# Optimization experiments

Hardware: AMD Instinct MI355X
Metric: run time of the kernel (lower is better)

Reference implementation:

```python
import jax, jax.numpy as jnp
import numpy as np

N, E, G, H, F_IN = 100_000, 3_200_000, 256, 16, 7
RRELU_SLOPE = (1.0 / 8.0 + 1.0 / 3.0) / 2.0  # eval-mode RReLU uses mean slope


def rrelu(x):
    return jnp.where(x >= 0, x, RRELU_SLOPE * x)


def gcn_conv(x, edge_index, edge_weight, W, b, n_nodes):
    """PyG GCNConv: add self-loops, symmetric norm, gather-matmul-scatter."""
    row, col = edge_index[0], edge_index[1]
    loop = jnp.arange(n_nodes)
    row = jnp.concatenate([row, loop])
    col = jnp.concatenate([col, loop])
    w = jnp.concatenate([edge_weight, jnp.ones((n_nodes,), x.dtype)])
    deg = jax.ops.segment_sum(w, col, num_segments=n_nodes)
    dis = jnp.where(deg > 0, jax.lax.rsqrt(jnp.maximum(deg, 1e-12)), 0.0)
    norm = dis[row] * w * dis[col]            # [E+N]
    h = x @ W                                  # [N, out]
    msg = h[row] * norm[:, None]               # gather + scale
    return jax.ops.segment_sum(msg, col, num_segments=n_nodes) + b


def max_pool_neighbor_x(x, edge_index, n_nodes):
    row, col = edge_index[0], edge_index[1]
    loop = jnp.arange(n_nodes)
    row = jnp.concatenate([row, loop])
    col = jnp.concatenate([col, loop])
    return jax.ops.segment_max(x[row], col, num_segments=n_nodes)


def setup_inputs() -> dict:
    key = jax.random.key(0)
    ks = jax.random.split(key, 12)
    x = jax.random.normal(ks[0], (N, F_IN), jnp.float32)
    edge_index = jax.random.randint(ks[1], (2, E), 0, N)
    edge_weights = jax.random.uniform(ks[2], (E,), jnp.float32)
    batch = (jnp.arange(N) * G) // N  # sorted, every graph non-empty
    s = 0.2
    W1 = jax.random.normal(ks[3], (F_IN, H), jnp.float32) * s
    b1 = jnp.zeros((H,), jnp.float32)
    W2 = jax.random.normal(ks[4], (H, H), jnp.float32) * s
    b2 = jnp.zeros((H,), jnp.float32)
    Wl1 = jax.random.normal(ks[5], (H, H), jnp.float32) * s
    bl1 = jax.random.normal(ks[6], (H,), jnp.float32) * s
    Wl3 = jax.random.normal(ks[7], (H, H), jnp.float32) * s
    bl3 = jax.random.normal(ks[8], (H,), jnp.float32) * s
    Wl4 = jax.random.normal(ks[9], (H, 1), jnp.float32) * s
    bl4 = jax.random.normal(ks[10], (1,), jnp.float32) * s
    return {"x": x, "edge_index": edge_index, "batch": batch,
            "edge_weights": edge_weights, "W1": W1, "b1": b1, "W2": W2,
            "b2": b2, "Wl1": Wl1, "bl1": bl1, "Wl3": Wl3, "bl3": bl3,
            "Wl4": Wl4, "bl4": bl4}


def reference(x, edge_index, batch, edge_weights, W1, b1, W2, b2,
              Wl1, bl1, Wl3, bl3, Wl4, bl4):
    h = gcn_conv(x, edge_index, edge_weights, W1, b1, N)
    h = max_pool_neighbor_x(h, edge_index, N)
    res = h
    h = gcn_conv(h, edge_index, jnp.ones((E,), h.dtype), W2, b2, N)
    h = jax.nn.relu(res + h)
    g = jax.ops.segment_max(h, batch, num_segments=G)  # global_max_pool
    res = g
    g = rrelu(res + (g @ Wl1 + bl1))
    res = g
    g = rrelu(res + (g @ Wl3 + bl3))
    # dropout p=0.5 in eval mode -> identity
    g = rrelu(g @ Wl4 + bl4)
    return g
```

## Files before the change

kernel.cpp:

```cpp
#include <hip/hip_runtime.h>
#include <hip/hip_fp16.h>
#include <math.h>

#define NN 100000
#define NE 3200000
#define NG 256
#define HD 16
#define FIN 7

#define RB 8
#define RSZ 256
#define NBUK 391
#define FB 1024
#define CHUNK 3125
#define ASTRIDE 17
#define CSTRIDE 9
#define LMASK 0x1FFFF

#define S16 65536.0f
#define INV_S16 1.52587890625e-5f
#define IBIAS 33554432u
#define S_DEGW 16777216.0f
#define INV_S_DEGW 5.9604644775390625e-8f

static constexpr float SLOPE = 0.22916666666666666f;

__device__ __forceinline__ float rrelu_f(float a) {
    return a >= 0.f ? a : SLOPE * a;
}

__device__ __forceinline__ unsigned encf(float v) {
    unsigned u = __float_as_uint(v);
    return u ^ (((unsigned)((int)u >> 31)) | 0x80000000u);
}
__device__ __forceinline__ float decf(unsigned u) {
    unsigned m = ((int)u < 0) ? 0x80000000u : 0xFFFFFFFFu;
    return __uint_as_float(u ^ m);
}
#define ENC_NEGINF 0x00800000u

__global__ __launch_bounds__(256) void k_node_prep(
        const float* __restrict__ x, const float* __restrict__ W1,
        float* __restrict__ h1) {
    int t = blockIdx.x * 256 + threadIdx.x;
    if (t >= NN * HD) return;
    int i = t >> 4, f = t & 15;
    float acc = 0.f;
#pragma unroll
    for (int k = 0; k < FIN; ++k) acc += x[i * FIN + k] * W1[k * HD + f];
    h1[t] = acc;
}

__global__ __launch_bounds__(256) void k_hist(
        const int* __restrict__ col, int* __restrict__ hist) {
    __shared__ int bins[NBUK];
    for (int i = threadIdx.x; i < NBUK; i += 256) bins[i] = 0;
    __syncthreads();
    int base = blockIdx.x * CHUNK;
    for (int i = threadIdx.x; i < CHUNK; i += 256)
        atomicAdd(&bins[col[base + i] >> RB], 1);
    __syncthreads();
    for (int i = threadIdx.x; i < NBUK; i += 256)
        hist[blockIdx.x * NBUK + i] = bins[i];
}

__global__ __launch_bounds__(FB) void k_scan_a(
        const int* __restrict__ hist, int* __restrict__ pre, int* __restrict__ tot) {
    __shared__ int s[FB];
    int t = threadIdx.x;
    int v = hist[t * NBUK + blockIdx.x];
    s[t] = v;
    __syncthreads();
    for (int d = 1; d < FB; d <<= 1) {
        int add = (t >= d) ? s[t - d] : 0;
        __syncthreads();
        s[t] += add;
        __syncthreads();
    }
    pre[blockIdx.x * FB + t] = s[t] - v;
    if (t == FB - 1) tot[blockIdx.x] = s[t];
}

__global__ __launch_bounds__(512) void k_scan_b(
        const int* __restrict__ tot, int* __restrict__ bstart) {
    __shared__ int s[512];
    int t = threadIdx.x;
    int v = (t < NBUK) ? tot[t] : 0;
    s[t] = v;
    __syncthreads();
    for (int d = 1; d < 512; d <<= 1) {
        int add = (t >= d) ? s[t - d] : 0;
        __syncthreads();
        s[t] += add;
        __syncthreads();
    }
    if (t < NBUK) bstart[t + 1] = s[t];
    if (t == 0) bstart[0] = 0;
}

__global__ __launch_bounds__(256) void k_fill(
        const int* __restrict__ row, const int* __restrict__ col,
        const float* __restrict__ ew,
        const int* __restrict__ pre, const int* __restrict__ bstart,
        uint2* __restrict__ spw) {
    __shared__ int lcnt[NBUK];
    __shared__ int gofs[NBUK];
    __shared__ int part[256];
    __shared__ unsigned short sbuk[CHUNK];
    __shared__ uint2 stage[CHUNK];
    int t = threadIdx.x;
    for (int i = t; i < NBUK; i += 256) {
        lcnt[i] = 0;
        gofs[i] = bstart[i] + pre[i * FB + blockIdx.x];
    }
    __syncthreads();
    int base = blockIdx.x * CHUNK;
    for (int i = t; i < CHUNK; i += 256)
        atomicAdd(&lcnt[col[base + i] >> RB], 1);
    __syncthreads();
    int k0 = t * 2;
    int c0 = (k0 + 0 < NBUK) ? lcnt[k0 + 0] : 0;
    int c1 = (k0 + 1 < NBUK) ? lcnt[k0 + 1] : 0;
    int gsum = c0 + c1;
    part[t] = gsum;
    __syncthreads();
    for (int d = 1; d < 256; d <<= 1) {
        int add = (t >= d) ? part[t - d] : 0;
        __syncthreads();
        part[t] += add;
        __syncthreads();
    }
    {
        int run = part[t] - gsum;
        int e0 = run, e1 = run + c0;
        if (k0 + 0 < NBUK) { gofs[k0 + 0] -= e0; lcnt[k0 + 0] = e0; }
        if (k0 + 1 < NBUK) { gofs[k0 + 1] -= e1; lcnt[k0 + 1] = e1; }
    }
    __syncthreads();
    for (int i = t; i < CHUNK; i += 256) {
        int c = col[base + i];
        int b = c >> RB;
        int s = atomicAdd(&lcnt[b], 1);
        stage[s] = make_uint2(((unsigned)(c & (RSZ - 1)) << 17) | (unsigned)row[base + i],
                              __float_as_uint(ew[base + i]));
        sbuk[s] = (unsigned short)b;
    }
    __syncthreads();
    for (int s = t; s < CHUNK; s += 256)
        spw[s + gofs[sbuk[s]]] = stage[s];
}

__global__ __launch_bounds__(1024) void k_deg(
        const uint2* __restrict__ spw, const int* __restrict__ bstart,
        const float* __restrict__ h1,
        float* __restrict__ dis1, float* __restrict__ dis2,
        int* __restrict__ cnts, unsigned* __restrict__ h1h) {
    __shared__ unsigned long long sdeg[RSZ];
    __shared__ float sdis[RSZ];
    int t = threadIdx.x;
    if (t < RSZ) sdeg[t] = 0ULL;
    __syncthreads();
    int s0 = bstart[blockIdx.x], s1 = bstart[blockIdx.x + 1];
    int j = s0 + t;
    for (; j + 3072 < s1; j += 4096) {
        uint2 e0 = spw[j], e1 = spw[j + 1024], e2 = spw[j + 2048], e3 = spw[j + 3072];
        atomicAdd(&sdeg[e0.x >> 17], (1ULL << 32) |
                  (unsigned long long)(unsigned)__float2int_rn(__uint_as_float(e0.y) * S_DEGW));
        atomicAdd(&sdeg[e1.x >> 17], (1ULL << 32) |
                  (unsigned long long)(unsigned)__float2int_rn(__uint_as_float(e1.y) * S_DEGW));
        atomicAdd(&sdeg[e2.x >> 17], (1ULL << 32) |
                  (unsigned long long)(unsigned)__float2int_rn(__uint_as_float(e2.y) * S_DEGW));
        atomicAdd(&sdeg[e3.x >> 17], (1ULL << 32) |
                  (unsigned long long)(unsigned)__float2int_rn(__uint_as_float(e3.y) * S_DEGW));
    }
    for (; j < s1; j += 1024) {
        uint2 e = spw[j];
        atomicAdd(&sdeg[e.x >> 17], (1ULL << 32) |
                  (unsigned long long)(unsigned)__float2int_rn(__uint_as_float(e.y) * S_DEGW));
    }
    __syncthreads();
    int node0 = blockIdx.x * RSZ;
    if (t < RSZ && node0 + t < NN) {
        unsigned long long v = sdeg[t];
        unsigned cnt = (unsigned)(v >> 32);
        float wsum = (float)(unsigned)(v & 0xFFFFFFFFULL) * INV_S_DEGW;
        float d1 = rsqrtf(wsum + 1.f);
        dis1[node0 + t] = d1;
        sdis[t] = d1;
        dis2[node0 + t] = rsqrtf((float)cnt + 1.f);
        cnts[node0 + t] = (int)cnt;
    }
    __syncthreads();
    for (int i = t; i < RSZ * 8; i += 1024) {
        int ln = i >> 3, p = i & 7;
        int node = node0 + ln;
        if (node < NN) {
            float d = sdis[ln];
            __half2 hh = __floats2half2_rn(h1[node * HD + 2 * p] * d,
                                           h1[node * HD + 2 * p + 1] * d);
            h1h[node * 8 + p] = *(unsigned*)&hh;
        }
    }
}

__device__ __forceinline__ void conv_acc(unsigned long long* acc, unsigned ex,
                                         unsigned g, float w, int p) {
    float2 f = __half22float2(*(__half2*)&g);
    unsigned q0 = (unsigned)__float2int_rn(f.x * w) + IBIAS;
    unsigned q1 = (unsigned)__float2int_rn(f.y * w) + IBIAS;
    atomicAdd(&acc[(ex >> 17) * CSTRIDE + p],
              ((unsigned long long)q0 << 32) | (unsigned long long)q1);
}

__global__ __launch_bounds__(1024) void k_conv1(
        const uint2* __restrict__ spw, const int* __restrict__ bstart,
        const unsigned* __restrict__ h1h, const float* __restrict__ h1,
        const float* __restrict__ dis1, const int* __restrict__ cnts,
        const float* __restrict__ b1, unsigned* __restrict__ h1outh) {
    __shared__ unsigned long long acc[RSZ * CSTRIDE];
    int t = threadIdx.x;
    for (int i = t; i < RSZ * CSTRIDE; i += 1024) acc[i] = 0ULL;
    __syncthreads();
    int p = t & 7, slot = t >> 3;
    int s0 = bstart[blockIdx.x], s1 = bstart[blockIdx.x + 1];
    int j = s0 + slot;
    for (; j + 384 < s1; j += 512) {
        uint2 e0 = spw[j], e1 = spw[j + 128], e2 = spw[j + 256], e3 = spw[j + 384];
        unsigned g0 = h1h[(e0.x & LMASK) * 8 + p];
        unsigned g1 = h1h[(e1.x & LMASK) * 8 + p];
        unsigned g2 = h1h[(e2.x & LMASK) * 8 + p];
        unsigned g3 = h1h[(e3.x & LMASK) * 8 + p];
        conv_acc(acc, e0.x, g0, __uint_as_float(e0.y) * S16, p);
        conv_acc(acc, e1.x, g1, __uint_as_float(e1.y) * S16, p);
        conv_acc(acc, e2.x, g2, __uint_as_float(e2.y) * S16, p);
        conv_acc(acc, e3.x, g3, __uint_as_float(e3.y) * S16, p);
    }
    for (; j < s1; j += 128) {
        uint2 e = spw[j];
        unsigned g = h1h[(e.x & LMASK) * 8 + p];
        conv_acc(acc, e.x, g, __uint_as_float(e.y) * S16, p);
    }
    __syncthreads();
    int node0 = blockIdx.x * RSZ;
    for (int i = t; i < RSZ * 8; i += 1024) {
        int ln = i >> 3, pp = i & 7;
        int node = node0 + ln;
        if (node < NN) {
            unsigned long long v = acc[ln * CSTRIDE + pp];
            unsigned kb = (unsigned)cnts[node] * IBIAS;
            float a0 = (float)(int)((unsigned)(v >> 32) - kb) * INV_S16;
            float a1 = (float)(int)((unsigned)(v & 0xFFFFFFFFULL) - kb) * INV_S16;
            float d = dis1[node];
            float r0 = a0 * d + h1[node * HD + 2 * pp] * d * d + b1[2 * pp];
            float r1 = a1 * d + h1[node * HD + 2 * pp + 1] * d * d + b1[2 * pp + 1];
            __half2 hh = __floats2half2_rn(r0, r1);
            h1outh[node * 8 + pp] = *(unsigned*)&hh;
        }
    }
}

__global__ __launch_bounds__(1024) void k_pool_h2(
        const uint2* __restrict__ spw, const int* __restrict__ bstart,
        const unsigned* __restrict__ h1outh, const float* __restrict__ W2,
        const float* __restrict__ dis2,
        float2* __restrict__ pool2, float2* __restrict__ h2s,
        unsigned* __restrict__ h2sh) {
    __shared__ unsigned acc[RSZ * ASTRIDE];
    __shared__ float sW2[256];
    int t = threadIdx.x;
    if (t < 256) sW2[t] = W2[t];
    for (int i = t; i < RSZ * ASTRIDE; i += 1024) acc[i] = ENC_NEGINF;
    __syncthreads();
    int p = t & 7, slot = t >> 3;
    int s0 = bstart[blockIdx.x], s1 = bstart[blockIdx.x + 1];
    int j = s0 + slot;
    for (; j + 384 < s1; j += 512) {
        unsigned e0 = spw[j].x, e1 = spw[j + 128].x, e2 = spw[j + 256].x, e3 = spw[j + 384].x;
        unsigned g0 = h1outh[(e0 & LMASK) * 8 + p];
        unsigned g1 = h1outh[(e1 & LMASK) * 8 + p];
        unsigned g2 = h1outh[(e2 & LMASK) * 8 + p];
        unsigned g3 = h1outh[(e3 & LMASK) * 8 + p];
        float2 f;
        f = __half22float2(*(__half2*)&g0);
        atomicMax(&acc[(e0 >> 17) * ASTRIDE + 2 * p], encf(f.x));
        atomicMax(&acc[(e0 >> 17) * ASTRIDE + 2 * p + 1], encf(f.y));
        f = __half22float2(*(__half2*)&g1);
        atomicMax(&acc[(e1 >> 17) * ASTRIDE + 2 * p], encf(f.x));
        atomicMax(&acc[(e1 >> 17) * ASTRIDE + 2 * p + 1], encf(f.y));
        f = __half22float2(*(__half2*)&g2);
        atomicMax(&acc[(e2 >> 17) * ASTRIDE + 2 * p], encf(f.x));
        atomicMax(&acc[(e2 >> 17) * ASTRIDE + 2 * p + 1], encf(f.y));
        f = __half22float2(*(__half2*)&g3);
        atomicMax(&acc[(e3 >> 17) * ASTRIDE + 2 * p], encf(f.x));
        atomicMax(&acc[(e3 >> 17) * ASTRIDE + 2 * p + 1], encf(f.y));
    }
    for (; j < s1; j += 128) {
        unsigned e = spw[j].x;
        unsigned g = h1outh[(e & LMASK) * 8 + p];
        float2 f = __half22float2(*(__half2*)&g);
        atomicMax(&acc[(e >> 17) * ASTRIDE + 2 * p], encf(f.x));
        atomicMax(&acc[(e >> 17) * ASTRIDE + 2 * p + 1], encf(f.y));
    }
    __syncthreads();
    int node0 = blockIdx.x * RSZ;
    for (int i = t; i < RSZ * 8; i += 1024) {
        int ln = i >> 3, pp = i & 7;
        int node = node0 + ln;
        if (node < NN) {
            unsigned sh = h1outh[node * 8 + pp];
            float2 sf = __half22float2(*(__half2*)&sh);
            float m0 = fmaxf(decf(acc[ln * ASTRIDE + 2 * pp]),     sf.x);
            float m1 = fmaxf(decf(acc[ln * ASTRIDE + 2 * pp + 1]), sf.y);
            pool2[node * 8 + pp] = make_float2(m0, m1);
            acc[ln * ASTRIDE + 2 * pp]     = __float_as_uint(m0);
            acc[ln * ASTRIDE + 2 * pp + 1] = __float_as_uint(m1);
        }
    }
    __syncthreads();
    for (int i = t; i < RSZ * 8; i += 1024) {
        int ln = i >> 3, pp = i & 7;
        int node = node0 + ln;
        if (node < NN) {
            float a0 = 0.f, a1 = 0.f;
#pragma unroll
            for (int k = 0; k < HD; ++k) {
                float pv = __uint_as_float(acc[ln * ASTRIDE + k]);
                a0 += pv * sW2[k * HD + 2 * pp];
                a1 += pv * sW2[k * HD + 2 * pp + 1];
            }
            float d = dis2[node];
            a0 *= d; a1 *= d;
            h2s[node * 8 + pp] = make_float2(a0, a1);
            __half2 hh = __floats2half2_rn(a0, a1);
            h2sh[node * 8 + pp] = *(unsigned*)&hh;
        }
    }
}

__global__ __launch_bounds__(1024) void k_conv2(
        const uint2* __restrict__ spw, const int* __restrict__ bstart,
        const unsigned* __restrict__ h2sh, const float2* __restrict__ h2s,
        const float* __restrict__ dis2, const int* __restrict__ cnts,
        const float2* __restrict__ pool2, const float* __restrict__ b2,
        float2* __restrict__ hfin2) {
    __shared__ unsigned long long acc[RSZ * CSTRIDE];
    int t = threadIdx.x;
    for (int i = t; i < RSZ * CSTRIDE; i += 1024) acc[i] = 0ULL;
    __syncthreads();
    int p = t & 7, slot = t >> 3;
    int s0 = bstart[blockIdx.x], s1 = bstart[blockIdx.x + 1];
    int j = s0 + slot;
    for (; j + 384 < s1; j += 512) {
        unsigned e0 = spw[j].x, e1 = spw[j + 128].x, e2 = spw[j + 256].x, e3 = spw[j + 384].x;
        unsigned g0 = h2sh[(e0 & LMASK) * 8 + p];
        unsigned g1 = h2sh[(e1 & LMASK) * 8 + p];
        unsigned g2 = h2sh[(e2 & LMASK) * 8 + p];
        unsigned g3 = h2sh[(e3 & LMASK) * 8 + p];
        conv_acc(acc, e0, g0, S16, p);
        conv_acc(acc, e1, g1, S16, p);
        conv_acc(acc, e2, g2, S16, p);
        conv_acc(acc, e3, g3, S16, p);
    }
    for (; j < s1; j += 128) {
        unsigned e = spw[j].x;
        unsigned g = h2sh[(e & LMASK) * 8 + p];
        conv_acc(acc, e, g, S16, p);
    }
    __syncthreads();
    int node0 = blockIdx.x * RSZ;
    for (int i = t; i < RSZ * 8; i += 1024) {
        int ln = i >> 3, pp = i & 7;
        int node = node0 + ln;
        if (node < NN) {
            unsigned long long v = acc[ln * CSTRIDE + pp];
            unsigned kb = (unsigned)cnts[node] * IBIAS;
            float a0 = (float)(int)((unsigned)(v >> 32) - kb) * INV_S16;
            float a1 = (float)(int)((unsigned)(v & 0xFFFFFFFFULL) - kb) * INV_S16;
            float d = dis2[node];
            float2 self = h2s[node * 8 + pp];
            float2 pl = pool2[node * 8 + pp];
            float r0 = pl.x + (a0 + self.x) * d + b2[2 * pp];
            float r1 = pl.y + (a1 + self.y) * d + b2[2 * pp + 1];
            hfin2[node * 8 + pp] = make_float2(fmaxf(r0, 0.f), fmaxf(r1, 0.f));
        }
    }
}

__global__ __launch_bounds__(256) void k_graph_max(
        const float* __restrict__ hfin, float* __restrict__ gbuf) {
    int g = blockIdx.x;
    int start = (g * NN + NG - 1) / NG;
    int end   = ((g + 1) * NN + NG - 1) / NG;
    int f = threadIdx.x & 15, sub = threadIdx.x >> 4;
    float m = -3.402823466e38f;
    for (int i = start + sub; i < end; i += 16)
        m = fmaxf(m, hfin[i * HD + f]);
    __shared__ float lds[256];
    lds[threadIdx.x] = m;
    __syncthreads();
    if (threadIdx.x < 16) {
        float mm = lds[threadIdx.x];
#pragma unroll
        for (int s = 1; s < 16; ++s) mm = fmaxf(mm, lds[s * 16 + threadIdx.x]);
        gbuf[g * HD + threadIdx.x] = mm;
    }
}

__global__ __launch_bounds__(256) void k_mlp(
        const float* __restrict__ gbuf,
        const float* __restrict__ Wl1, const float* __restrict__ bl1,
        const float* __restrict__ Wl3, const float* __restrict__ bl3,
        const float* __restrict__ Wl4, const float* __restrict__ bl4,
        float* __restrict__ out) {
    __shared__ float sW1[256], sW3[256], sW4[16], sb1[16], sb3[16];
    __shared__ float sb4;
    int tid = threadIdx.x;
    sW1[tid] = Wl1[tid];
    sW3[tid] = Wl3[tid];
    if (tid < 16) { sW4[tid] = Wl4[tid]; sb1[tid] = bl1[tid]; sb3[tid] = bl3[tid]; }
    if (tid == 0) sb4 = bl4[0];
    __syncthreads();

    float v[16], t1[16], t2[16];
#pragma unroll
    for (int f = 0; f < 16; ++f) v[f] = gbuf[tid * 16 + f];
#pragma unroll
    for (int f = 0; f < 16; ++f) {
        float a = sb1[f] + v[f];
#pragma unroll
        for (int k = 0; k < 16; ++k) a += v[k] * sW1[k * 16 + f];
        t1[f] = rrelu_f(a);
    }
#pragma unroll
    for (int f = 0; f < 16; ++f) {
        float a = sb3[f] + t1[f];
#pragma unroll
        for (int k = 0; k < 16; ++k) a += t1[k] * sW3[k * 16 + f];
        t2[f] = rrelu_f(a);
    }
    float o = sb4;
#pragma unroll
    for (int k = 0; k < 16; ++k) o += t2[k] * sW4[k];
    out[tid] = rrelu_f(o);
}

extern "C" void kernel_launch(void* const* d_in, const int* in_sizes, int n_in,
                              void* d_out, int out_size, void* d_ws, size_t ws_size,
                              hipStream_t stream) {
    const float* x   = (const float*)d_in[0];
    const int*   ei  = (const int*)  d_in[1];
    const float* ew  = (const float*)d_in[3];
    const float* W1  = (const float*)d_in[4];
    const float* b1  = (const float*)d_in[5];
    const float* W2  = (const float*)d_in[6];
    const float* b2  = (const float*)d_in[7];
    const float* Wl1 = (const float*)d_in[8];
    const float* bl1 = (const float*)d_in[9];
    const float* Wl3 = (const float*)d_in[10];
    const float* bl3 = (const float*)d_in[11];
    const float* Wl4 = (const float*)d_in[12];
    const float* bl4 = (const float*)d_in[13];
    const int* row = ei;
    const int* col = ei + NE;

    float* ws = (float*)d_ws;
    float* h1    = ws;
    float* pool  = h1   + NN * HD;
    float* h2s   = pool + NN * HD;
    float* dis1  = h2s  + NN * HD;
    float* dis2  = dis1 + NN;
    int*   cnts  = (int*)(dis2 + NN);
    float* gbuf  = (float*)(cnts + NN);
    unsigned* h1h    = (unsigned*)(gbuf + NG * HD);
    unsigned* h1outh = h1h    + NN * 8;
    unsigned* h2sh   = h1outh + NN * 8;
    uint2*    spw    = (uint2*)(h2sh + NN * 8);
    int* tot    = (int*)(spw + NE);
    int* bstart = tot + NBUK;
    int* hist   = (int*)pool;
    int* pre    = (int*)h2s;
    float* hfin = h1;

    const int B = 256;

    k_node_prep<<<(NN * HD + B - 1) / B, B, 0, stream>>>(x, W1, h1);
    k_hist     <<<FB, B, 0, stream>>>(col, hist);
    k_scan_a   <<<NBUK, FB, 0, stream>>>(hist, pre, tot);
    k_scan_b   <<<1, 512, 0, stream>>>(tot, bstart);
    k_fill     <<<FB, B, 0, stream>>>(row, col, ew, pre, bstart, spw);
    k_deg      <<<NBUK, 1024, 0, stream>>>(spw, bstart, h1, dis1, dis2, cnts, h1h);
    k_conv1    <<<NBUK, 1024, 0, stream>>>(spw, bstart, h1h, h1, dis1, cnts, b1, h1outh);
    k_pool_h2  <<<NBUK, 1024, 0, stream>>>(spw, bstart, h1outh, W2, dis2,
                                           (float2*)pool, (float2*)h2s, h2sh);
    k_conv2    <<<NBUK, 1024, 0, stream>>>(spw, bstart, h2sh, (const float2*)h2s, dis2,
                                           cnts, (const float2*)pool, b2, (float2*)hfin);
    k_graph_max<<<NG, B, 0, stream>>>(hfin, gbuf);
    k_mlp      <<<1, B, 0, stream>>>(gbuf, Wl1, bl1, Wl3, bl3, Wl4, bl4, (float*)d_out);
}
```

Baseline: 266.4 us.

## Split edge records into index and fp16 weight arrays, widen gathers, fuse node prep

Stores sorted edges as a 32-bit packed index array plus a separate fp16 weight array instead of 8-byte uint2 records, shrinking edge traffic in every pass (conv2 and pool no longer read weights at all). Gather kernels now have each thread load 8-byte uint2 feature chunks (4 threads per edge) and issue paired atomics. The x@W1 node prep is fused into k_deg, and the bucket scan is rewritten to process 8 columns per block with a transposed layout and wavefront shuffles. Converting edge weights to fp16 adds rounding error to degrees and messages.

```diff
diff --git a/kernel.cpp b/kernel.cpp
--- a/kernel.cpp
+++ b/kernel.cpp
@@ -11,8 +11,10 @@
 #define RB 8
 #define RSZ 256
 #define NBUK 391
+#define NBUKP 400
 #define FB 1024
 #define CHUNK 3125
+#define SCB 8
 #define ASTRIDE 17
 #define CSTRIDE 9
 #define LMASK 0x1FFFF
@@ -39,16 +41,9 @@
 }
 #define ENC_NEGINF 0x00800000u
 
-__global__ __launch_bounds__(256) void k_node_prep(
-        const float* __restrict__ x, const float* __restrict__ W1,
-        float* __restrict__ h1) {
-    int t = blockIdx.x * 256 + threadIdx.x;
-    if (t >= NN * HD) return;
-    int i = t >> 4, f = t & 15;
-    float acc = 0.f;
-#pragma unroll
-    for (int k = 0; k < FIN; ++k) acc += x[i * FIN + k] * W1[k * HD + f];
-    h1[t] = acc;
+__device__ __forceinline__ float h2f(unsigned short us) {
+    __half h = *(__half*)&us;
+    return __half2float(h);
 }
 
 __global__ __launch_bounds__(256) void k_hist(
@@ -61,24 +56,47 @@
         atomicAdd(&bins[col[base + i] >> RB], 1);
     __syncthreads();
     for (int i = threadIdx.x; i < NBUK; i += 256)
-        hist[blockIdx.x * NBUK + i] = bins[i];
-}
-
-__global__ __launch_bounds__(FB) void k_scan_a(
-        const int* __restrict__ hist, int* __restrict__ pre, int* __restrict__ tot) {
-    __shared__ int s[FB];
-    int t = threadIdx.x;
-    int v = hist[t * NBUK + blockIdx.x];
-    s[t] = v;
-    __syncthreads();
-    for (int d = 1; d < FB; d <<= 1) {
-        int add = (t >= d) ? s[t - d] : 0;
-        __syncthreads();
-        s[t] += add;
-        __syncthreads();
-    }
-    pre[blockIdx.x * FB + t] = s[t] - v;
-    if (t == FB - 1) tot[blockIdx.x] = s[t];
+        hist[blockIdx.x * NBUKP + i] = bins[i];
+}
+
+__global__ __launch_bounds__(512) void k_scan_a(
+        const int* __restrict__ hist, int* __restrict__ pre_t,
+        int* __restrict__ tot) {
+    __shared__ int s[SCB * (FB + 1)];
+    int t = threadIdx.x;
+    int c0 = blockIdx.x * SCB;
+    for (int i = t; i < SCB * FB; i += 512) {
+        int j = i >> 3, c = i & 7;
+        int cc = c0 + c;
+        s[c * (FB + 1) + j] = (cc < NBUK) ? hist[j * NBUKP + cc] : 0;
+    }
+    __syncthreads();
+    int w = t >> 6, l = t & 63;
+    int* sb = &s[w * (FB + 1)];
+    int base = l * 16;
+    int loc[16];
+    int run = 0;
+#pragma unroll
+    for (int k = 0; k < 16; ++k) { loc[k] = run; run += sb[base + k]; }
+    int inc = run;
+#pragma unroll
+    for (int d = 1; d < 64; d <<= 1) {
+        int v = __shfl_up(inc, d, 64);
+        if (l >= d) inc += v;
+    }
+    int excl = inc - run;
+    int cc = c0 + w;
+    if (cc < NBUK) {
+#pragma unroll
+        for (int k = 0; k < 16; ++k) sb[base + k] = excl + loc[k];
+        if (l == 63) tot[cc] = inc;
+    }
+    __syncthreads();
+    for (int i = t; i < SCB * FB; i += 512) {
+        int j = i >> 3, c = i & 7;
+        int cc2 = c0 + c;
+        if (cc2 < NBUK) pre_t[j * NBUKP + cc2] = s[c * (FB + 1) + j];
+    }
 }
 
 __global__ __launch_bounds__(512) void k_scan_b(
@@ -101,17 +119,18 @@
 __global__ __launch_bounds__(256) void k_fill(
         const int* __restrict__ row, const int* __restrict__ col,
         const float* __restrict__ ew,
-        const int* __restrict__ pre, const int* __restrict__ bstart,
-        uint2* __restrict__ spw) {
+        const int* __restrict__ pre_t, const int* __restrict__ bstart,
+        unsigned* __restrict__ sp, unsigned short* __restrict__ swh) {
     __shared__ int lcnt[NBUK];
     __shared__ int gofs[NBUK];
     __shared__ int part[256];
+    __shared__ unsigned ssp[CHUNK];
+    __shared__ unsigned short ssw[CHUNK];
     __shared__ unsigned short sbuk[CHUNK];
-    __shared__ uint2 stage[CHUNK];
     int t = threadIdx.x;
     for (int i = t; i < NBUK; i += 256) {
         lcnt[i] = 0;
-        gofs[i] = bstart[i] + pre[i * FB + blockIdx.x];
+        gofs[i] = bstart[i] + pre_t[blockIdx.x * NBUKP + i];
     }
     __syncthreads();
     int base = blockIdx.x * CHUNK;
@@ -141,42 +160,53 @@
         int c = col[base + i];
         int b = c >> RB;
         int s = atomicAdd(&lcnt[b], 1);
-        stage[s] = make_uint2(((unsigned)(c & (RSZ - 1)) << 17) | (unsigned)row[base + i],
-                              __float_as_uint(ew[base + i]));
+        ssp[s] = ((unsigned)(c & (RSZ - 1)) << 17) | (unsigned)row[base + i];
+        __half hv = __float2half_rn(ew[base + i]);
+        ssw[s] = *(unsigned short*)&hv;
         sbuk[s] = (unsigned short)b;
     }
     __syncthreads();
-    for (int s = t; s < CHUNK; s += 256)
-        spw[s + gofs[sbuk[s]]] = stage[s];
+    for (int s = t; s < CHUNK; s += 256) {
+        int g = s + gofs[sbuk[s]];
+        sp[g] = ssp[s];
+        swh[g] = ssw[s];
+    }
 }
 
 __global__ __launch_bounds__(1024) void k_deg(
-        const uint2* __restrict__ spw, const int* __restrict__ bstart,
-        const float* __restrict__ h1,
-        float* __restrict__ dis1, float* __restrict__ dis2,
-        int* __restrict__ cnts, unsigned* __restrict__ h1h) {
+        const unsigned* __restrict__ sp, const unsigned short* __restrict__ swh,
+        const int* __restrict__ bstart,
+        const float* __restrict__ x, const float* __restrict__ W1,
+        float* __restrict__ h1, float* __restrict__ dis1,
+        float* __restrict__ dis2, int* __restrict__ cnts,
+        unsigned* __restrict__ h1h) {
     __shared__ unsigned long long sdeg[RSZ];
     __shared__ float sdis[RSZ];
-    int t = threadIdx.x;
+    __shared__ float sW1[FIN * HD];
+    int t = threadIdx.x;
+    if (t < FIN * HD) sW1[t] = W1[t];
     if (t < RSZ) sdeg[t] = 0ULL;
     __syncthreads();
     int s0 = bstart[blockIdx.x], s1 = bstart[blockIdx.x + 1];
     int j = s0 + t;
     for (; j + 3072 < s1; j += 4096) {
-        uint2 e0 = spw[j], e1 = spw[j + 1024], e2 = spw[j + 2048], e3 = spw[j + 3072];
-        atomicAdd(&sdeg[e0.x >> 17], (1ULL << 32) |
-                  (unsigned long long)(unsigned)__float2int_rn(__uint_as_float(e0.y) * S_DEGW));
-        atomicAdd(&sdeg[e1.x >> 17], (1ULL << 32) |
-                  (unsigned long long)(unsigned)__float2int_rn(__uint_as_float(e1.y) * S_DEGW));
-        atomicAdd(&sdeg[e2.x >> 17], (1ULL << 32) |
-                  (unsigned long long)(unsigned)__float2int_rn(__uint_as_float(e2.y) * S_DEGW));
-        atomicAdd(&sdeg[e3.x >> 17], (1ULL << 32) |
-                  (unsigned long long)(unsigned)__float2int_rn(__uint_as_float(e3.y) * S_DEGW));
+        unsigned e0 = sp[j], e1 = sp[j + 1024], e2 = sp[j + 2048], e3 = sp[j + 3072];
+        float w0 = h2f(swh[j]), w1 = h2f(swh[j + 1024]);
+        float w2 = h2f(swh[j + 2048]), w3 = h2f(swh[j + 3072]);
+        atomicAdd(&sdeg[e0 >> 17], (1ULL << 32) |
+                  (unsigned long long)(unsigned)__float2int_rn(w0 * S_DEGW));
+        atomicAdd(&sdeg[e1 >> 17], (1ULL << 32) |
+                  (unsigned long long)(unsigned)__float2int_rn(w1 * S_DEGW));
+        atomicAdd(&sdeg[e2 >> 17], (1ULL << 32) |
+                  (unsigned long long)(unsigned)__float2int_rn(w2 * S_DEGW));
+        atomicAdd(&sdeg[e3 >> 17], (1ULL << 32) |
+                  (unsigned long long)(unsigned)__float2int_rn(w3 * S_DEGW));
     }
     for (; j < s1; j += 1024) {
-        uint2 e = spw[j];
-        atomicAdd(&sdeg[e.x >> 17], (1ULL << 32) |
-                  (unsigned long long)(unsigned)__float2int_rn(__uint_as_float(e.y) * S_DEGW));
+        unsigned e = sp[j];
+        float w = h2f(swh[j]);
+        atomicAdd(&sdeg[e >> 17], (1ULL << 32) |
+                  (unsigned long long)(unsigned)__float2int_rn(w * S_DEGW));
     }
     __syncthreads();
     int node0 = blockIdx.x * RSZ;
@@ -195,25 +225,40 @@
         int ln = i >> 3, p = i & 7;
         int node = node0 + ln;
         if (node < NN) {
+            float a0 = 0.f, a1 = 0.f;
+#pragma unroll
+            for (int k = 0; k < FIN; ++k) {
+                float xv = x[node * FIN + k];
+                a0 += xv * sW1[k * HD + 2 * p];
+                a1 += xv * sW1[k * HD + 2 * p + 1];
+            }
+            h1[node * HD + 2 * p] = a0;
+            h1[node * HD + 2 * p + 1] = a1;
             float d = sdis[ln];
-            __half2 hh = __floats2half2_rn(h1[node * HD + 2 * p] * d,
-                                           h1[node * HD + 2 * p + 1] * d);
+            __half2 hh = __floats2half2_rn(a0 * d, a1 * d);
             h1h[node * 8 + p] = *(unsigned*)&hh;
         }
     }
 }
 
-__device__ __forceinline__ void conv_acc(unsigned long long* acc, unsigned ex,
-                                         unsigned g, float w, int p) {
-    float2 f = __half22float2(*(__half2*)&g);
-    unsigned q0 = (unsigned)__float2int_rn(f.x * w) + IBIAS;
-    unsigned q1 = (unsigned)__float2int_rn(f.y * w) + IBIAS;
-    atomicAdd(&acc[(ex >> 17) * CSTRIDE + p],
-              ((unsigned long long)q0 << 32) | (unsigned long long)q1);
+__device__ __forceinline__ void conv_acc2(unsigned long long* acc, unsigned ex,
+                                          uint2 g, float w, int p2) {
+    float2 fa = __half22float2(*(__half2*)&g.x);
+    float2 fb = __half22float2(*(__half2*)&g.y);
+    unsigned qa0 = (unsigned)__float2int_rn(fa.x * w) + IBIAS;
+    unsigned qa1 = (unsigned)__float2int_rn(fa.y * w) + IBIAS;
+    unsigned qb0 = (unsigned)__float2int_rn(fb.x * w) + IBIAS;
+    unsigned qb1 = (unsigned)__float2int_rn(fb.y * w) + IBIAS;
+    int lc = ex >> 17;
+    atomicAdd(&acc[lc * CSTRIDE + 2 * p2],
+              ((unsigned long long)qa0 << 32) | (unsigned long long)qa1);
+    atomicAdd(&acc[lc * CSTRIDE + 2 * p2 + 1],
+              ((unsigned long long)qb0 << 32) | (unsigned long long)qb1);
 }
 
 __global__ __launch_bounds__(1024) void k_conv1(
-        const uint2* __restrict__ spw, const int* __restrict__ bstart,
+        const unsigned* __restrict__ sp, const unsigned short* __restrict__ swh,
+        const int* __restrict__ bstart,
         const unsigned* __restrict__ h1h, const float* __restrict__ h1,
         const float* __restrict__ dis1, const int* __restrict__ cnts,
         const float* __restrict__ b1, unsigned* __restrict__ h1outh) {
@@ -221,24 +266,28 @@
     int t = threadIdx.x;
     for (int i = t; i < RSZ * CSTRIDE; i += 1024) acc[i] = 0ULL;
     __syncthreads();
-    int p = t & 7, slot = t >> 3;
+    int p2 = t & 3, slot = t >> 2;
+    const uint2* h1h2 = (const uint2*)h1h;
     int s0 = bstart[blockIdx.x], s1 = bstart[blockIdx.x + 1];
     int j = s0 + slot;
-    for (; j + 384 < s1; j += 512) {
-        uint2 e0 = spw[j], e1 = spw[j + 128], e2 = spw[j + 256], e3 = spw[j + 384];
-        unsigned g0 = h1h[(e0.x & LMASK) * 8 + p];
-        unsigned g1 = h1h[(e1.x & LMASK) * 8 + p];
-        unsigned g2 = h1h[(e2.x & LMASK) * 8 + p];
-        unsigned g3 = h1h[(e3.x & LMASK) * 8 + p];
-        conv_acc(acc, e0.x, g0, __uint_as_float(e0.y) * S16, p);
-        conv_acc(acc, e1.x, g1, __uint_as_float(e1.y) * S16, p);
-        conv_acc(acc, e2.x, g2, __uint_as_float(e2.y) * S16, p);
-        conv_acc(acc, e3.x, g3, __uint_as_float(e3.y) * S16, p);
-    }
-    for (; j < s1; j += 128) {
-        uint2 e = spw[j];
-        unsigned g = h1h[(e.x & LMASK) * 8 + p];
-        conv_acc(acc, e.x, g, __uint_as_float(e.y) * S16, p);
+    for (; j + 768 < s1; j += 1024) {
+        unsigned e0 = sp[j], e1 = sp[j + 256], e2 = sp[j + 512], e3 = sp[j + 768];
+        float w0 = h2f(swh[j]) * S16, w1 = h2f(swh[j + 256]) * S16;
+        float w2 = h2f(swh[j + 512]) * S16, w3 = h2f(swh[j + 768]) * S16;
+        uint2 g0 = h1h2[(e0 & LMASK) * 4 + p2];
+        uint2 g1 = h1h2[(e1 & LMASK) * 4 + p2];
+        uint2 g2 = h1h2[(e2 & LMASK) * 4 + p2];
+        uint2 g3 = h1h2[(e3 & LMASK) * 4 + p2];
+        conv_acc2(acc, e0, g0, w0, p2);
+        conv_acc2(acc, e1, g1, w1, p2);
+        conv_acc2(acc, e2, g2, w2, p2);
+        conv_acc2(acc, e3, g3, w3, p2);
+    }
+    for (; j < s1; j += 256) {
+        unsigned e = sp[j];
+        float w = h2f(swh[j]) * S16;
+        uint2 g = h1h2[(e & LMASK) * 4 + p2];
+        conv_acc2(acc, e, g, w, p2);
     }
     __syncthreads();
     int node0 = blockIdx.x * RSZ;
@@ -260,7 +309,7 @@
 }
 
 __global__ __launch_bounds__(1024) void k_pool_h2(
-        const uint2* __restrict__ spw, const int* __restrict__ bstart,
+        const unsigned* __restrict__ sp, const int* __restrict__ bstart,
         const unsigned* __restrict__ h1outh, const float* __restrict__ W2,
         const float* __restrict__ dis2,
         float2* __restrict__ pool2, float2* __restrict__ h2s,
@@ -271,35 +320,47 @@
     if (t < 256) sW2[t] = W2[t];
     for (int i = t; i < RSZ * ASTRIDE; i += 1024) acc[i] = ENC_NEGINF;
     __syncthreads();
-    int p = t & 7, slot = t >> 3;
+    int p2 = t & 3, slot = t >> 2;
+    const uint2* hv2 = (const uint2*)h1outh;
     int s0 = bstart[blockIdx.x], s1 = bstart[blockIdx.x + 1];
     int j = s0 + slot;
-    for (; j + 384 < s1; j += 512) {
-        unsigned e0 = spw[j].x, e1 = spw[j + 128].x, e2 = spw[j + 256].x, e3 = spw[j + 384].x;
-        unsigned g0 = h1outh[(e0 & LMASK) * 8 + p];
-        unsigned g1 = h1outh[(e1 & LMASK) * 8 + p];
-        unsigned g2 = h1outh[(e2 & LMASK) * 8 + p];
-        unsigned g3 = h1outh[(e3 & LMASK) * 8 + p];
+    for (; j + 768 < s1; j += 1024) {
+        unsigned e0 = sp[j], e1 = sp[j + 256], e2 = sp[j + 512], e3 = sp[j + 768];
+        uint2 g0 = hv2[(e0 & LMASK) * 4 + p2];
+        uint2 g1 = hv2[(e1 & LMASK) * 4 + p2];
+        uint2 g2 = hv2[(e2 & LMASK) * 4 + p2];
+        uint2 g3 = hv2[(e3 & LMASK) * 4 + p2];
         float2 f;
-        f = __half22float2(*(__half2*)&g0);
-        atomicMax(&acc[(e0 >> 17) * ASTRIDE + 2 * p], encf(f.x));
-        atomicMax(&acc[(e0 >> 17) * ASTRIDE + 2 * p + 1], encf(f.y));
-        f = __half22float2(*(__half2*)&g1);
-        atomicMax(&acc[(e1 >> 17) * ASTRIDE + 2 * p], encf(f.x));
-        atomicMax(&acc[(e1 >> 17) * ASTRIDE + 2 * p + 1], encf(f.y));
-        f = __half22float2(*(__half2*)&g2);
-        atomicMax(&acc[(e2 >> 17) * ASTRIDE + 2 * p], encf(f.x));
-        atomicMax(&acc[(e2 >> 17) * ASTRIDE + 2 * p + 1], encf(f.y));
-        f = __half22float2(*(__half2*)&g3);
-        atomicMax(&acc[(e3 >> 17) * ASTRIDE + 2 * p], encf(f.x));
-        atomicMax(&acc[(e3 >> 17) * ASTRIDE + 2 * p + 1], encf(f.y));
-    }
-    for (; j < s1; j += 128) {
-        unsigned e = spw[j].x;
-        unsigned g = h1outh[(e & LMASK) * 8 + p];
-        float2 f = __half22float2(*(__half2*)&g);
-        atomicMax(&acc[(e >> 17) * ASTRIDE + 2 * p], encf(f.x));
-        atomicMax(&acc[(e >> 17) * ASTRIDE + 2 * p + 1], encf(f.y));
+        unsigned* a;
+        a = &acc[(e0 >> 17) * ASTRIDE + 4 * p2];
+        f = __half22float2(*(__half2*)&g0.x);
+        atomicMax(a + 0, encf(f.x)); atomicMax(a + 1, encf(f.y));
+        f = __half22float2(*(__half2*)&g0.y);
+        atomicMax(a + 2, encf(f.x)); atomicMax(a + 3, encf(f.y));
+        a = &acc[(e1 >> 17) * ASTRIDE + 4 * p2];
+        f = __half22float2(*(__half2*)&g1.x);
+        atomicMax(a + 0, encf(f.x)); atomicMax(a + 1, encf(f.y));
+        f = __half22float2(*(__half2*)&g1.y);
+        atomicMax(a + 2, encf(f.x)); atomicMax(a + 3, encf(f.y));
+        a = &acc[(e2 >> 17) * ASTRIDE + 4 * p2];
+        f = __half22float2(*(__half2*)&g2.x);
+        atomicMax(a + 0, encf(f.x)); atomicMax(a + 1, encf(f.y));
+        f = __half22float2(*(__half2*)&g2.y);
+        atomicMax(a + 2, encf(f.x)); atomicMax(a + 3, encf(f.y));
+        a = &acc[(e3 >> 17) * ASTRIDE + 4 * p2];
+        f = __half22float2(*(__half2*)&g3.x);
+        atomicMax(a + 0, encf(f.x)); atomicMax(a + 1, encf(f.y));
+        f = __half22float2(*(__half2*)&g3.y);
+        atomicMax(a + 2, encf(f.x)); atomicMax(a + 3, encf(f.y));
+    }
+    for (; j < s1; j += 256) {
+        unsigned e = sp[j];
+        uint2 g = hv2[(e & LMASK) * 4 + p2];
+        unsigned* a = &acc[(e >> 17) * ASTRIDE + 4 * p2];
+        float2 f = __half22float2(*(__half2*)&g.x);
+        atomicMax(a + 0, encf(f.x)); atomicMax(a + 1, encf(f.y));
+        f = __half22float2(*(__half2*)&g.y);
+        atomicMax(a + 2, encf(f.x)); atomicMax(a + 3, encf(f.y));
     }
     __syncthreads();
     int node0 = blockIdx.x * RSZ;
@@ -338,7 +399,7 @@
 }
 
 __global__ __launch_bounds__(1024) void k_conv2(
-        const uint2* __restrict__ spw, const int* __restrict__ bstart,
+        const unsigned* __restrict__ sp, const int* __restrict__ bstart,
         const unsigned* __restrict__ h2sh, const float2* __restrict__ h2s,
         const float* __restrict__ dis2, const int* __restrict__ cnts,
         const float2* __restrict__ pool2, const float* __restrict__ b2,
@@ -347,24 +408,25 @@
     int t = threadIdx.x;
     for (int i = t; i < RSZ * CSTRIDE; i += 1024) acc[i] = 0ULL;
     __syncthreads();
-    int p = t & 7, slot = t >> 3;
+    int p2 = t & 3, slot = t >> 2;
+    const uint2* hv2 = (const uint2*)h2sh;
     int s0 = bstart[blockIdx.x], s1 = bstart[blockIdx.x + 1];
     int j = s0 + slot;
-    for (; j + 384 < s1; j += 512) {
-        unsigned e0 = spw[j].x, e1 = spw[j + 128].x, e2 = spw[j + 256].x, e3 = spw[j + 384].x;
-        unsigned g0 = h2sh[(e0 & LMASK) * 8 + p];
-        unsigned g1 = h2sh[(e1 & LMASK) * 8 + p];
-        unsigned g2 = h2sh[(e2 & LMASK) * 8 + p];
-        unsigned g3 = h2sh[(e3 & LMASK) * 8 + p];
-        conv_acc(acc, e0, g0, S16, p);
-        conv_acc(acc, e1, g1, S16, p);
-        conv_acc(acc, e2, g2, S16, p);
-        conv_acc(acc, e3, g3, S16, p);
-    }
-    for (; j < s1; j += 128) {
-        unsigned e = spw[j].x;
-        unsigned g = h2sh[(e & LMASK) * 8 + p];
-        conv_acc(acc, e, g, S16, p);
+    for (; j + 768 < s1; j += 1024) {
+        unsigned e0 = sp[j], e1 = sp[j + 256], e2 = sp[j + 512], e3 = sp[j + 768];
+        uint2 g0 = hv2[(e0 & LMASK) * 4 + p2];
+        uint2 g1 = hv2[(e1 & LMASK) * 4 + p2];
+        uint2 g2 = hv2[(e2 & LMASK) * 4 + p2];
+        uint2 g3 = hv2[(e3 & LMASK) * 4 + p2];
+        conv_acc2(acc, e0, g0, S16, p2);
+        conv_acc2(acc, e1, g1, S16, p2);
+        conv_acc2(acc, e2, g2, S16, p2);
+        conv_acc2(acc, e3, g3, S16, p2);
+    }
+    for (; j < s1; j += 256) {
+        unsigned e = sp[j];
+        uint2 g = hv2[(e & LMASK) * 4 + p2];
+        conv_acc2(acc, e, g, S16, p2);
     }
     __syncthreads();
     int node0 = blockIdx.x * RSZ;
@@ -474,25 +536,27 @@
     unsigned* h1h    = (unsigned*)(gbuf + NG * HD);
     unsigned* h1outh = h1h    + NN * 8;
     unsigned* h2sh   = h1outh + NN * 8;
-    uint2*    spw    = (uint2*)(h2sh + NN * 8);
-    int* tot    = (int*)(spw + NE);
+    unsigned* sp     = h2sh   + NN * 8;
+    unsigned short* swh = (unsigned short*)(sp + NE);
+    int* tot    = (int*)(swh + NE + (NE & 1));
     int* bstart = tot + NBUK;
     int* hist   = (int*)pool;
-    int* pre    = (int*)h2s;
+    int* pre_t  = (int*)h2s;
     float* hfin = h1;
 
     const int B = 256;
 
-    k_node_prep<<<(NN * HD + B - 1) / B, B, 0, stream>>>(x, W1, h1);
     k_hist     <<<FB, B, 0, stream>>>(col, hist);
-    k_scan_a   <<<NBUK, FB, 0, stream>>>(hist, pre, tot);
+    k_scan_a   <<<(NBUK + SCB - 1) / SCB, 512, 0, stream>>>(hist, pre_t, tot);
     k_scan_b   <<<1, 512, 0, stream>>>(tot, bstart);
-    k_fill     <<<FB, B, 0, stream>>>(row, col, ew, pre, bstart, spw);
-    k_deg      <<<NBUK, 1024, 0, stream>>>(spw, bstart, h1, dis1, dis2, cnts, h1h);
-    k_conv1    <<<NBUK, 1024, 0, stream>>>(spw, bstart, h1h, h1, dis1, cnts, b1, h1outh);
-    k_pool_h2  <<<NBUK, 1024, 0, stream>>>(spw, bstart, h1outh, W2, dis2,
+    k_fill     <<<FB, B, 0, stream>>>(row, col, ew, pre_t, bstart, sp, swh);
+    k_deg      <<<NBUK, 1024, 0, stream>>>(sp, swh, bstart, x, W1, h1,
+                                           dis1, dis2, cnts, h1h);
+    k_conv1    <<<NBUK, 1024, 0, stream>>>(sp, swh, bstart, h1h, h1, dis1,
+                                           cnts, b1, h1outh);
+    k_pool_h2  <<<NBUK, 1024, 0, stream>>>(sp, bstart, h1outh, W2, dis2,
                                            (float2*)pool, (float2*)h2s, h2sh);
-    k_conv2    <<<NBUK, 1024, 0, stream>>>(spw, bstart, h2sh, (const float2*)h2s, dis2,
+    k_conv2    <<<NBUK, 1024, 0, stream>>>(sp, bstart, h2sh, (const float2*)h2s, dis2,
                                            cnts, (const float2*)pool, b2, (float2*)hfin);
     k_graph_max<<<NG, B, 0, stream>>>(hfin, gbuf);
     k_mlp      <<<1, B, 0, stream>>>(gbuf, Wl1, bl1, Wl3, bl3, Wl4, bl4, (float*)d_out);
```

New measurement: 259.5 us. 2.6% less time.
